# Kernel tuning notes

Hardware: AMD Instinct MI355X
Metric: run time of the kernel (lower is better)

The kernel has to match this reference:

```python
import jax, jax.numpy as jnp
import numpy as np

B, L, T = 16, 256, 256
ENC, DEC, MEL, SPK = 256, 1024, 80, 256
ATT, FILT, K = 128, 32, 31


def setup_inputs() -> dict:
    key = jax.random.key(0)
    ks = jax.random.split(key, 32)
    s = 0.05
    r = lambda k, shape: jax.random.normal(k, shape, dtype=jnp.float32) * s
    return {
        'encoder_outputs': jax.random.normal(ks[0], (B, L, ENC), dtype=jnp.float32),
        'speaker_embed': jax.random.normal(ks[1], (B, SPK), dtype=jnp.float32),
        'mels': jax.random.normal(ks[2], (B, T, MEL), dtype=jnp.float32),
        # prenet
        'W_pre1': r(ks[3], (DEC, MEL)), 'b_pre1': jnp.zeros((DEC,), jnp.float32),
        'W_pre2': r(ks[4], (DEC, DEC)), 'b_pre2': jnp.zeros((DEC,), jnp.float32),
        # speaker projection
        'W_sp': r(ks[5], (DEC, SPK)), 'b_sp': jnp.zeros((DEC,), jnp.float32),
        # location-sensitive attention (Tacotron-2 style)
        'W_q': r(ks[6], (ATT, DEC)),
        'W_m': r(ks[7], (ATT, ENC)),
        'W_loc_conv': r(ks[8], (FILT, 2, K)),
        'W_loc': r(ks[9], (ATT, FILT)),
        'v_att': r(ks[10], (ATT,)),
        # LSTM cells
        'W_ih1': r(ks[11], (4 * DEC, DEC + ENC)), 'W_hh1': r(ks[12], (4 * DEC, DEC)),
        'b_ih1': jnp.zeros((4 * DEC,), jnp.float32), 'b_hh1': jnp.zeros((4 * DEC,), jnp.float32),
        'W_ih2': r(ks[13], (4 * DEC, DEC)), 'W_hh2': r(ks[14], (4 * DEC, DEC)),
        'b_ih2': jnp.zeros((4 * DEC,), jnp.float32), 'b_hh2': jnp.zeros((4 * DEC,), jnp.float32),
        # output projections
        'W_mel': r(ks[15], (MEL, DEC)), 'b_mel': jnp.zeros((MEL,), jnp.float32),
        'W_stop': r(ks[16], (1, DEC)), 'b_stop': jnp.zeros((1,), jnp.float32),
    }


def _lstm_cell(x, h, c, W_ih, W_hh, b_ih, b_hh):
    g = x @ W_ih.T + h @ W_hh.T + b_ih + b_hh
    i, f, gg, o = jnp.split(g, 4, axis=-1)
    c2 = jax.nn.sigmoid(f) * c + jax.nn.sigmoid(i) * jnp.tanh(gg)
    h2 = jax.nn.sigmoid(o) * jnp.tanh(c2)
    return h2, c2


def reference(encoder_outputs, speaker_embed, mels,
              W_pre1, b_pre1, W_pre2, b_pre2, W_sp, b_sp,
              W_q, W_m, W_loc_conv, W_loc, v_att,
              W_ih1, W_hh1, b_ih1, b_hh1, W_ih2, W_hh2, b_ih2, b_hh2,
              W_mel, b_mel, W_stop, b_stop):
    b = encoder_outputs.shape[0]
    proc_mem = jnp.einsum('bld,ad->bla', encoder_outputs, W_m)  # [B,L,ATT]
    spk = speaker_embed @ W_sp.T + b_sp                          # [B,DEC]
    # teacher forcing: step 0 uses zeros, step i>0 uses mels[:, i] (matches torch loop)
    prev_mel_seq = jnp.concatenate([jnp.zeros_like(mels[:, :1]), mels[:, 1:]], axis=1)
    prev_mel_seq = prev_mel_seq.transpose(1, 0, 2)               # [T,B,MEL]

    def step(carry, prev_mel):
        h1, c1, h2, c2, prev_w, cum_w = carry
        # prenet (dropout = identity in eval)
        p = jax.nn.relu(prev_mel @ W_pre1.T + b_pre1)
        p = jax.nn.relu(p @ W_pre2.T + b_pre2)
        q = p + spk
        # location features over [prev, cumulative] attention weights
        loc = jnp.stack([prev_w, cum_w], axis=1)                 # [B,2,L]
        f = jax.lax.conv_general_dilated(loc, W_loc_conv, (1,), [(K // 2, K // 2)],
                                         dimension_numbers=('NCH', 'OIH', 'NCH'))  # [B,FILT,L]
        e = jnp.einsum('bla,a->bl', jnp.tanh((q @ W_q.T)[:, None, :]
                                             + jnp.einsum('bcl,ac->bla', f, W_loc)
                                             + proc_mem), v_att)  # [B,L]
        w = jax.nn.softmax(e, axis=1)
        ctx = jnp.einsum('bl,bld->bd', w, encoder_outputs)        # [B,ENC]
        h1n, c1n = _lstm_cell(jnp.concatenate([p, ctx], axis=1), h1, c1, W_ih1, W_hh1, b_ih1, b_hh1)
        h2n, c2n = _lstm_cell(h1n, h2, c2, W_ih2, W_hh2, b_ih2, b_hh2)
        mel = h2n @ W_mel.T + b_mel
        stop = jax.nn.sigmoid(h2n @ W_stop.T + b_stop)
        return (h1n, c1n, h2n, c2n, w, cum_w + w), (mel, stop)

    z = lambda d: jnp.zeros((b, d), jnp.float32)
    carry0 = (z(DEC), z(DEC), z(DEC), z(DEC), z(L), z(L))
    _, (mel_seq, stop_seq) = jax.lax.scan(step, carry0, prev_mel_seq)
    return mel_seq.transpose(1, 0, 2), stop_seq.transpose(1, 0, 2)
```

## Files before the change

### kernel.cpp

```cpp
#include <hip/hip_runtime.h>


namespace {

constexpr int TT = 256, BB = 16, LL = 256, MELD = 80, FILTD = 32, KC = 31;
constexpr int P1 = 2308;
constexpr int P2 = 2052;

typedef float f32x4 __attribute__((ext_vector_type(4)));

struct Args {
  const float *enc, *spe, *mels;
  const float *Wpre1, *bpre1, *Wpre2, *bpre2, *Wsp, *bsp;
  const float *Wq, *Wm, *Wconv, *Wloc, *vatt;
  const float *Wih1, *Whh1, *bih1, *bhh1;
  const float *Wih2, *Whh2, *bih2, *bhh2;
  const float *Wmel, *bmel, *Wstop, *bstop;
  float *p, *X, *qp2, *pm2, *prevmel;
  float *h1a, *h1b, *c1, *h2a, *h2b, *c2;
  float *cum, *wexp, *uctx, *pctx, *psum, *spkvec, *spkq;
  float *W81, *b81, *tmp;
  int *slots, *epoch, *pslots, *pepoch;
  float *out;
};

__device__ __forceinline__ float fast_tanh(float x) {
  float ax = fabsf(x);
  float e = __expf(-2.f * ax);
  float t = (1.f - e) / (1.f + e);
  return copysignf(t, x);
}
__device__ __forceinline__ float fast_sig(float x) { return 1.f / (1.f + __expf(-x)); }

__device__ __forceinline__ float cld1(const float* p) {
  float v;
  asm volatile("global_load_dword %0, %1, off sc0 sc1\n\ts_waitcnt vmcnt(0)"
               : "=v"(v) : "v"(p) : "memory");
  return v;
}
__device__ __forceinline__ int cldi(const int* p) {
  int v;
  asm volatile("global_load_dword %0, %1, off sc0 sc1\n\ts_waitcnt vmcnt(0)"
               : "=v"(v) : "v"(p) : "memory");
  return v;
}
__device__ __forceinline__ void cst1(float* p, float v) {
  asm volatile("global_store_dword %0, %1, off sc0 sc1" :: "v"(p), "v"(v) : "memory");
}
__device__ __forceinline__ void csti(int* p, int v) {
  asm volatile("global_store_dword %0, %1, off sc0 sc1" :: "v"(p), "v"(v) : "memory");
}
__device__ __forceinline__ void cld4(f32x4 d[4], const f32x4* q0, const f32x4* q1,
                                     const f32x4* q2, const f32x4* q3) {
  asm volatile(
      "global_load_dwordx4 %0, %4, off sc0 sc1\n\t"
      "global_load_dwordx4 %1, %5, off sc0 sc1\n\t"
      "global_load_dwordx4 %2, %6, off sc0 sc1\n\t"
      "global_load_dwordx4 %3, %7, off sc0 sc1\n\t"
      "s_waitcnt vmcnt(0)"
      : "=&v"(d[0]), "=&v"(d[1]), "=&v"(d[2]), "=&v"(d[3])
      : "v"(q0), "v"(q1), "v"(q2), "v"(q3)
      : "memory");
}
__device__ __forceinline__ void cld8(f32x4 d[8], const f32x4* q0, const f32x4* q1,
                                     const f32x4* q2, const f32x4* q3, const f32x4* q4,
                                     const f32x4* q5, const f32x4* q6, const f32x4* q7) {
  asm volatile(
      "global_load_dwordx4 %0, %8, off sc0 sc1\n\t"
      "global_load_dwordx4 %1, %9, off sc0 sc1\n\t"
      "global_load_dwordx4 %2, %10, off sc0 sc1\n\t"
      "global_load_dwordx4 %3, %11, off sc0 sc1\n\t"
      "global_load_dwordx4 %4, %12, off sc0 sc1\n\t"
      "global_load_dwordx4 %5, %13, off sc0 sc1\n\t"
      "global_load_dwordx4 %6, %14, off sc0 sc1\n\t"
      "global_load_dwordx4 %7, %15, off sc0 sc1\n\t"
      "s_waitcnt vmcnt(0)"
      : "=&v"(d[0]), "=&v"(d[1]), "=&v"(d[2]), "=&v"(d[3]),
        "=&v"(d[4]), "=&v"(d[5]), "=&v"(d[6]), "=&v"(d[7])
      : "v"(q0), "v"(q1), "v"(q2), "v"(q3), "v"(q4), "v"(q5), "v"(q6), "v"(q7)
      : "memory");
}
__device__ __forceinline__ void cld8d(float d[8], const float* q0, const float* q1,
                                      const float* q2, const float* q3, const float* q4,
                                      const float* q5, const float* q6, const float* q7) {
  asm volatile(
      "global_load_dword %0, %8, off sc0 sc1\n\t"
      "global_load_dword %1, %9, off sc0 sc1\n\t"
      "global_load_dword %2, %10, off sc0 sc1\n\t"
      "global_load_dword %3, %11, off sc0 sc1\n\t"
      "global_load_dword %4, %12, off sc0 sc1\n\t"
      "global_load_dword %5, %13, off sc0 sc1\n\t"
      "global_load_dword %6, %14, off sc0 sc1\n\t"
      "global_load_dword %7, %15, off sc0 sc1\n\t"
      "s_waitcnt vmcnt(0)"
      : "=&v"(d[0]), "=&v"(d[1]), "=&v"(d[2]), "=&v"(d[3]),
        "=&v"(d[4]), "=&v"(d[5]), "=&v"(d[6]), "=&v"(d[7])
      : "v"(q0), "v"(q1), "v"(q2), "v"(q3), "v"(q4), "v"(q5), "v"(q6), "v"(q7)
      : "memory");
}

__device__ __forceinline__ void gridbar(int* slots, int* epoch, int target) {
  __syncthreads();
  if (blockIdx.x == 0) {
    if (threadIdx.x == 0) csti(&slots[0], target);
    while (cldi(&slots[threadIdx.x * 32]) < target) __builtin_amdgcn_s_sleep(1);
    __syncthreads();
    if (threadIdx.x == 0) csti(epoch, target);
  } else {
    if (threadIdx.x == 0) {
      csti(&slots[blockIdx.x * 32], target);
      while (cldi(epoch) < target) __builtin_amdgcn_s_sleep(8);
    }
  }
  __syncthreads();
}

__global__ void k_init(float* base, int n) {
  int i = blockIdx.x * blockDim.x + threadIdx.x;
  if (i < n) base[i] = 0.f;
}

__global__ void k_setpsum(float* psum) {
  if (threadIdx.x < 16) psum[256 + threadIdx.x * 16] = 1.f;
}

__global__ void k_prevmel(Args a) {
  int i = blockIdx.x * blockDim.x + threadIdx.x;
  if (i >= TT * BB * MELD) return;
  int m = i % MELD;
  int tb = i / MELD;
  int b = tb & 15, t = tb >> 4;
  a.prevmel[i] = (t == 0) ? 0.f : a.mels[(b * TT + t) * MELD + m];
}

__global__ void k_spkvec(Args a) {
  int i = blockIdx.x * blockDim.x + threadIdx.x;
  if (i >= BB * 1024) return;
  int b = i >> 10, j = i & 1023;
  const float* x = a.spe + b * 256;
  const float* w = a.Wsp + j * 256;
  float s = a.bsp[j];
  for (int k = 0; k < 256; ++k) s += x[k] * w[k];
  a.spkvec[i] = s;
}

__global__ void k_spkq(Args a) {
  int i = blockIdx.x * blockDim.x + threadIdx.x;
  if (i >= BB * 128) return;
  int b = i >> 7, q = i & 127;
  const float* x = a.spkvec + b * 1024;
  const float* w = a.Wq + q * 1024;
  float s = 0.f;
  for (int k = 0; k < 1024; ++k) s += x[k] * w[k];
  a.spkq[i] = s;
}

__global__ void k_prep81(Args a) {
  int i = blockIdx.x * blockDim.x + threadIdx.x;
  if (i < 81 * 1024) {
    int r = i >> 10, k = i & 1023;
    a.W81[i] = (r < 80) ? a.Wmel[r * 1024 + k] : a.Wstop[k];
  }
  if (i < 81) a.b81[i] = (i < 80) ? a.bmel[i] : a.bstop[0];
}

__global__ __launch_bounds__(256) void k_gemm(const float* __restrict__ A,
                                              const float* __restrict__ Bm,
                                              const float* __restrict__ bias,
                                              float* __restrict__ C,
                                              int M, int N, int K, int act) {
  __shared__ __align__(16) float As[16][132];
  __shared__ __align__(16) float Bs[16][68];
  const int bm = blockIdx.y * 128, bn = blockIdx.x * 64;
  const int tid = threadIdx.x;
  const int tm = (tid >> 4) * 8, tn = (tid & 15) * 4;
  float acc[8][4] = {};
  for (int k0 = 0; k0 < K; k0 += 16) {
    for (int i = tid; i < 512; i += 256) {
      int m = i >> 2, kq = i & 3;
      float4 v = *(const float4*)(A + (size_t)(bm + m) * K + k0 + kq * 4);
      As[kq * 4 + 0][m] = v.x; As[kq * 4 + 1][m] = v.y;
      As[kq * 4 + 2][m] = v.z; As[kq * 4 + 3][m] = v.w;
    }
    {
      int m = tid >> 2, kq = tid & 3;
      float4 v = *(const float4*)(Bm + (size_t)(bn + m) * K + k0 + kq * 4);
      Bs[kq * 4 + 0][m] = v.x; Bs[kq * 4 + 1][m] = v.y;
      Bs[kq * 4 + 2][m] = v.z; Bs[kq * 4 + 3][m] = v.w;
    }
    __syncthreads();
#pragma unroll
    for (int kk = 0; kk < 16; ++kk) {
      float4 a0 = *(const float4*)&As[kk][tm];
      float4 a1 = *(const float4*)&As[kk][tm + 4];
      float4 b0 = *(const float4*)&Bs[kk][tn];
      float av[8] = {a0.x, a0.y, a0.z, a0.w, a1.x, a1.y, a1.z, a1.w};
      float bv[4] = {b0.x, b0.y, b0.z, b0.w};
#pragma unroll
      for (int i = 0; i < 8; ++i)
#pragma unroll
        for (int j = 0; j < 4; ++j) acc[i][j] += av[i] * bv[j];
    }
    __syncthreads();
  }
#pragma unroll
  for (int i = 0; i < 8; ++i)
#pragma unroll
    for (int j = 0; j < 4; ++j) {
      float v = acc[i][j];
      if (bias) v += bias[bn + tn + j];
      if (act == 1) v = fmaxf(v, 0.f);
      C[(size_t)(bm + tm + i) * N + bn + tn + j] = v;
    }
}

__global__ void k_pm_transpose(Args a) {
  int i = blockIdx.x * blockDim.x + threadIdx.x;
  if (i >= BB * 128 * LL) return;
  int l = i & 255;
  int rest = i >> 8;
  int q = rest & 127, b = rest >> 7;
  a.pm2[i] = a.X[(size_t)((b << 8) + l) * 128 + q];
}

__global__ void k_addspkq(Args a) {
  int i = blockIdx.x * blockDim.x + threadIdx.x;
  if (i >= TT * BB * 128) return;
  int q = i & 127, b = (i >> 7) & 15;
  a.qp2[i] += a.spkq[b * 128 + q];
}

__global__ __launch_bounds__(256, 1) void k_barprobe(Args a) {
  for (int t = 0; t < 512; ++t) gridbar(a.pslots, a.pepoch, t + 1);
}

__global__ __launch_bounds__(256, 1) void k_persist(Args a) {
  __shared__ __align__(16) float xs[16 * P1];
  __shared__ float gbuf[16][20];
  const int wg = blockIdx.x, tid = threadIdx.x;
  const int wv = tid >> 6, lane = tid & 63;
  const int d0 = wg * 4, kl = lane * 4;

  float4 wL1[9][4];
  float4 wL2[8][4];
#pragma unroll
  for (int q = 0; q < 4; ++q) {
    const int row = wv * 1024 + d0 + q;
    const float* rih1 = a.Wih1 + (size_t)row * 1280;
    const float* rhh1 = a.Whh1 + (size_t)row * 1024;
    const float* rih2 = a.Wih2 + (size_t)row * 1024;
    const float* rhh2 = a.Whh2 + (size_t)row * 1024;
#pragma unroll
    for (int kb = 0; kb < 9; ++kb)
      wL1[kb][q] = (kb < 5) ? *(const float4*)(rih1 + kb * 256 + kl)
                            : *(const float4*)(rhh1 + kb * 256 + kl - 1280);
#pragma unroll
    for (int kb = 0; kb < 8; ++kb)
      wL2[kb][q] = (kb < 4) ? *(const float4*)(rih2 + kb * 256 + kl)
                            : *(const float4*)(rhh2 + kb * 256 + kl - 1024);
  }
  const int row_r = wv * 1024 + d0 + (lane >> 4);
  const float bsum1 = a.bih1[row_r] + a.bhh1[row_r];
  const float bsum2 = a.bih2[row_r] + a.bhh2[row_r];

  for (int t = 0; t < 259; ++t) {
    const int cur = t & 1, prv = cur ^ 1;

    if (t < 256) {
      float* loc0 = xs;
      float* loc1 = xs + 64;
      float* F = xs + 128;
      float* expv = xs + 672;
      const int b = wg >> 4, c = wg & 15, l0 = c << 4;
      float sm;
      {
        const f32x4* ps4 = (const f32x4*)(a.psum + prv * 256 + b * 16);
        f32x4 pd[4];
        cld4(pd, ps4, ps4 + 1, ps4 + 2, ps4 + 3);
        sm = 0.f;
#pragma unroll
        for (int i = 0; i < 4; ++i) sm += pd[i][0] + pd[i][1] + pd[i][2] + pd[i][3];
      }
      const float inv_ps = 1.f / sm;
      if (tid < 64) {
        int lp = l0 - 16 + tid;
        bool ok = (lp >= 0 && lp < LL);
        float we = 0.f, cm = 0.f;
        if (ok) {
          we = cld1(a.wexp + prv * 4096 + b * 256 + lp) * inv_ps;
          cm = cld1(a.cum + prv * 4096 + b * 256 + lp);
        }
        loc0[tid] = we;
        loc1[tid] = ok ? (cm + we) : 0.f;
      }
      __syncthreads();
      if (tid < 16) cst1(a.cum + cur * 4096 + b * 256 + l0 + tid, loc1[16 + tid]);
      for (int idx = tid; idx < FILTD * 16; idx += 256) {
        int fc = idx >> 4, ll = idx & 15;
        const float* w = a.Wconv + fc * 62;
        float s = 0.f;
#pragma unroll
        for (int k = 0; k < KC; ++k) {
          s += w[k] * loc0[ll + k + 1];
          s += w[31 + k] * loc1[ll + k + 1];
        }
        F[fc * 17 + ll] = s;
      }
      __syncthreads();
      {
        const int ll = tid >> 4, ag = tid & 15;
        const int l = l0 + ll;
        const float* qpb = a.qp2 + (size_t)((t << 4) + b) * 128;
        const float* pmb = a.pm2 + (size_t)b * 128 * 256;
        float s = 0.f;
        for (int q = ag * 8; q < ag * 8 + 8; ++q) {
          float x = qpb[q] + pmb[q * 256 + l];
          const float* wl = a.Wloc + q * 32;
#pragma unroll
          for (int fc = 0; fc < FILTD; ++fc) x += wl[fc] * F[fc * 17 + ll];
          s += a.vatt[q] * fast_tanh(x);
        }
        s += __shfl_down(s, 8, 16);
        s += __shfl_down(s, 4, 16);
        s += __shfl_down(s, 2, 16);
        s += __shfl_down(s, 1, 16);
        if (ag == 0) {
          float ex = __expf(s);
          expv[ll] = ex;
          cst1(a.wexp + cur * 4096 + b * 256 + l, ex);
        }
      }
      __syncthreads();
      if (tid == 0) {
        float s = 0.f;
#pragma unroll
        for (int i = 0; i < 16; ++i) s += expv[i];
        cst1(a.psum + cur * 256 + b * 16 + c, s);
      }
      {
        float s = 0.f;
        const float* eb = a.enc + (size_t)((b << 8) + l0) * 256 + tid;
#pragma unroll
        for (int ll = 0; ll < 16; ++ll) s += expv[ll] * eb[ll * 256];
        cst1(a.pctx + cur * 65536 + (b * 16 + c) * 256 + tid, s);
      }
      __syncthreads();
    }

    if (wg < 16 && t >= 1 && t <= 256) {
      const int s = t - 1, par = s & 1, b = wg;
      float sm;
      {
        const f32x4* ps4 = (const f32x4*)(a.psum + par * 256 + b * 16);
        f32x4 pd[4];
        cld4(pd, ps4, ps4 + 1, ps4 + 2, ps4 + 3);
        sm = 0.f;
#pragma unroll
        for (int i = 0; i < 4; ++i) sm += pd[i][0] + pd[i][1] + pd[i][2] + pd[i][3];
      }
      const float inv = 1.f / sm;
      const float* pc = a.pctx + par * 65536 + b * 4096 + tid;
      float d[8];
      float acc = 0.f;
      cld8d(d, pc, pc + 256, pc + 512, pc + 768, pc + 1024, pc + 1280, pc + 1536,
            pc + 1792);
#pragma unroll
      for (int i = 0; i < 8; ++i) acc += d[i];
      cld8d(d, pc + 2048, pc + 2304, pc + 2560, pc + 2816, pc + 3072, pc + 3328,
            pc + 3584, pc + 3840);
#pragma unroll
      for (int i = 0; i < 8; ++i) acc += d[i];
      cst1(a.uctx + par * 4096 + b * 256 + tid, acc * inv);
    }

    if (t >= 2 && t <= 257) {
      const int s1 = t - 2;
      const float* pt = a.p + (size_t)s1 * 16384;
      const float* h1r = (s1 & 1) ? a.h1a : a.h1b;
      float* h1w = (s1 & 1) ? a.h1b : a.h1a;
      for (int k = 0; k < 16; ++k) {
        int i4 = tid + k * 256, b = i4 >> 8, kq = i4 & 255;
        *(f32x4*)(xs + b * P1 + kq * 4) = *(const f32x4*)(pt + (size_t)i4 * 4);
      }
      {
        const f32x4* q = (const f32x4*)(a.uctx + (size_t)(s1 & 1) * 4096);
        f32x4 d[4];
        cld4(d, q + tid, q + tid + 256, q + tid + 512, q + tid + 768);
#pragma unroll
        for (int k = 0; k < 4; ++k) {
          int i4 = tid + k * 256, b = i4 >> 6, kq = i4 & 63;
          *(f32x4*)(xs + b * P1 + 1024 + kq * 4) = d[k];
        }
      }
      {
        const f32x4* q = (const f32x4*)h1r;
        f32x4 d[8];
#pragma unroll
        for (int hb = 0; hb < 2; ++hb) {
          const f32x4* qq = q + tid + hb * 2048;
          cld8(d, qq, qq + 256, qq + 512, qq + 768, qq + 1024, qq + 1280, qq + 1536,
               qq + 1792);
#pragma unroll
          for (int k = 0; k < 8; ++k) {
            int i4 = tid + (hb * 8 + k) * 256, b = i4 >> 8, kq = i4 & 255;
            *(f32x4*)(xs + b * P1 + 1280 + kq * 4) = d[k];
          }
        }
      }
      __syncthreads();
      float acc[4][16];
#pragma unroll
      for (int q = 0; q < 4; ++q)
#pragma unroll
        for (int b = 0; b < 16; ++b) acc[q][b] = 0.f;
#pragma unroll
      for (int kb = 0; kb < 9; ++kb) {
        const float* xb = xs + kb * 256 + kl;
#pragma unroll
        for (int b = 0; b < 16; ++b) {
          float4 x4 = *(const float4*)(xb + b * P1);
#pragma unroll
          for (int q = 0; q < 4; ++q) {
            acc[q][b] += wL1[kb][q].x * x4.x;
            acc[q][b] += wL1[kb][q].y * x4.y;
            acc[q][b] += wL1[kb][q].z * x4.z;
            acc[q][b] += wL1[kb][q].w * x4.w;
          }
        }
      }
      __syncthreads();
      float* red = xs + wv * 4352;
#pragma unroll
      for (int q = 0; q < 4; ++q)
#pragma unroll
        for (int b = 0; b < 16; ++b) red[(q * 16 + b) * 68 + lane] = acc[q][b];
      __syncthreads();
      {
        const float* rr = xs + wv * 4352 + lane * 68;
        float4 s4 = {0.f, 0.f, 0.f, 0.f};
#pragma unroll
        for (int i = 0; i < 16; ++i) {
          float4 v = *(const float4*)(rr + i * 4);
          s4.x += v.x; s4.y += v.y; s4.z += v.z; s4.w += v.w;
        }
        gbuf[wv * 4 + (lane >> 4)][lane & 15] = s4.x + s4.y + s4.z + s4.w + bsum1;
      }
      __syncthreads();
      if (tid < 64) {
        int dd = tid >> 4, b = tid & 15;
        int d = d0 + dd;
        float gi = gbuf[0 + dd][b], gf = gbuf[4 + dd][b];
        float gg = gbuf[8 + dd][b], go = gbuf[12 + dd][b];
        float co = a.c1[b * 1024 + d];
        float cn = fast_sig(gf) * co + fast_sig(gi) * fast_tanh(gg);
        float hn = fast_sig(go) * fast_tanh(cn);
        a.c1[b * 1024 + d] = cn;
        cst1(h1w + b * 1024 + d, hn);
      }
      __syncthreads();
    }

    if (t >= 3) {
      const int s2 = t - 3;
      const float* h1s = (s2 & 1) ? a.h1b : a.h1a;
      const float* h2r = (s2 & 1) ? a.h2a : a.h2b;
      float* h2w = (s2 & 1) ? a.h2b : a.h2a;
      {
        f32x4 d[8];
        const f32x4* q1 = (const f32x4*)h1s;
        const f32x4* q2 = (const f32x4*)h2r;
#pragma unroll
        for (int hb = 0; hb < 2; ++hb) {
          const f32x4* qq = q1 + tid + hb * 2048;
          cld8(d, qq, qq + 256, qq + 512, qq + 768, qq + 1024, qq + 1280, qq + 1536,
               qq + 1792);
#pragma unroll
          for (int k = 0; k < 8; ++k) {
            int i4 = tid + (hb * 8 + k) * 256, b = i4 >> 8, kq = i4 & 255;
            *(f32x4*)(xs + b * P2 + kq * 4) = d[k];
          }
        }
#pragma unroll
        for (int hb = 0; hb < 2; ++hb) {
          const f32x4* qq = q2 + tid + hb * 2048;
          cld8(d, qq, qq + 256, qq + 512, qq + 768, qq + 1024, qq + 1280, qq + 1536,
               qq + 1792);
#pragma unroll
          for (int k = 0; k < 8; ++k) {
            int i4 = tid + (hb * 8 + k) * 256, b = i4 >> 8, kq = i4 & 255;
            *(f32x4*)(xs + b * P2 + 1024 + kq * 4) = d[k];
          }
        }
      }
      __syncthreads();
      float acc[4][16];
#pragma unroll
      for (int q = 0; q < 4; ++q)
#pragma unroll
        for (int b = 0; b < 16; ++b) acc[q][b] = 0.f;
#pragma unroll
      for (int kb = 0; kb < 8; ++kb) {
        const float* xb = xs + kb * 256 + kl;
#pragma unroll
        for (int b = 0; b < 16; ++b) {
          float4 x4 = *(const float4*)(xb + b * P2);
#pragma unroll
          for (int q = 0; q < 4; ++q) {
            acc[q][b] += wL2[kb][q].x * x4.x;
            acc[q][b] += wL2[kb][q].y * x4.y;
            acc[q][b] += wL2[kb][q].z * x4.z;
            acc[q][b] += wL2[kb][q].w * x4.w;
          }
        }
      }
      __syncthreads();
      float* red = xs + wv * 4352;
#pragma unroll
      for (int q = 0; q < 4; ++q)
#pragma unroll
        for (int b = 0; b < 16; ++b) red[(q * 16 + b) * 68 + lane] = acc[q][b];
      __syncthreads();
      {
        const float* rr = xs + wv * 4352 + lane * 68;
        float4 s4 = {0.f, 0.f, 0.f, 0.f};
#pragma unroll
        for (int i = 0; i < 16; ++i) {
          float4 v = *(const float4*)(rr + i * 4);
          s4.x += v.x; s4.y += v.y; s4.z += v.z; s4.w += v.w;
        }
        gbuf[wv * 4 + (lane >> 4)][lane & 15] = s4.x + s4.y + s4.z + s4.w + bsum2;
      }
      __syncthreads();
      if (tid < 64) {
        int dd = tid >> 4, b = tid & 15;
        int d = d0 + dd;
        float gi = gbuf[0 + dd][b], gf = gbuf[4 + dd][b];
        float gg = gbuf[8 + dd][b], go = gbuf[12 + dd][b];
        float co = a.c2[b * 1024 + d];
        float cn = fast_sig(gf) * co + fast_sig(gi) * fast_tanh(gg);
        float hn = fast_sig(go) * fast_tanh(cn);
        a.c2[b * 1024 + d] = cn;
        cst1(h2w + b * 1024 + d, hn);
        a.X[(size_t)(s2 * 16 + b) * 1024 + d] = hn;
      }
    }

    if (t < 258) gridbar(a.slots, a.epoch, t + 1);
  }
}

__global__ void k_finish(Args a) {
  int i = blockIdx.x * blockDim.x + threadIdx.x;
  if (i >= 4096 * 128) return;
  int col = i & 127, tb = i >> 7;
  int t = tb >> 4, b = tb & 15;
  float v = a.tmp[i];
  if (col < 80) a.out[(size_t)(b * 256 + t) * 80 + col] = v;
  else if (col == 80) a.out[327680 + b * 256 + t] = fast_sig(v);
}

}

extern "C" void kernel_launch(void* const* d_in, const int* in_sizes, int n_in,
                              void* d_out, int out_size, void* d_ws, size_t ws_size,
                              hipStream_t stream) {
  float* ws = (float*)d_ws;
  Args a;
  a.enc = (const float*)d_in[0];
  a.spe = (const float*)d_in[1];
  a.mels = (const float*)d_in[2];
  a.Wpre1 = (const float*)d_in[3];  a.bpre1 = (const float*)d_in[4];
  a.Wpre2 = (const float*)d_in[5];  a.bpre2 = (const float*)d_in[6];
  a.Wsp = (const float*)d_in[7];    a.bsp = (const float*)d_in[8];
  a.Wq = (const float*)d_in[9];     a.Wm = (const float*)d_in[10];
  a.Wconv = (const float*)d_in[11]; a.Wloc = (const float*)d_in[12];
  a.vatt = (const float*)d_in[13];
  a.Wih1 = (const float*)d_in[14];  a.Whh1 = (const float*)d_in[15];
  a.bih1 = (const float*)d_in[16];  a.bhh1 = (const float*)d_in[17];
  a.Wih2 = (const float*)d_in[18];  a.Whh2 = (const float*)d_in[19];
  a.bih2 = (const float*)d_in[20];  a.bhh2 = (const float*)d_in[21];
  a.Wmel = (const float*)d_in[22];  a.bmel = (const float*)d_in[23];
  a.Wstop = (const float*)d_in[24]; a.bstop = (const float*)d_in[25];

  a.p    = ws + 0;
  a.X    = ws + 4194304;
  a.qp2  = ws + 8388608;
  a.pm2  = ws + 8912896;
  float* st = ws + 9437184;
  a.h1a = st + 0;      a.h1b = st + 16384;
  a.c1  = st + 32768;
  a.h2a = st + 49152;  a.h2b = st + 65536;
  a.c2  = st + 81920;
  a.cum  = st + 98304;
  a.wexp = st + 106496;
  a.uctx = st + 114688;
  a.pctx = st + 122880;
  a.psum = st + 253952;
  a.slots  = (int*)(st + 254464);
  a.epoch  = (int*)(st + 262656);
  a.pslots = (int*)(st + 262688);
  a.pepoch = (int*)(st + 270880);
  a.spkvec = ws + 9708096;
  a.spkq   = ws + 9724480;
  a.W81    = ws + 9726528;
  a.b81    = ws + 9857600;
  a.tmp    = ws + 9857728;
  a.prevmel = a.tmp;
  a.out = (float*)d_out;

  k_init<<<(270912 + 255) / 256, 256, 0, stream>>>(st, 270912);
  k_setpsum<<<1, 64, 0, stream>>>(a.psum);
  k_prevmel<<<(TT * BB * MELD + 255) / 256, 256, 0, stream>>>(a);
  k_spkvec<<<(BB * 1024 + 255) / 256, 256, 0, stream>>>(a);
  k_spkq<<<(BB * 128 + 255) / 256, 256, 0, stream>>>(a);
  k_prep81<<<(81 * 1024 + 255) / 256, 256, 0, stream>>>(a);

  k_gemm<<<dim3(16, 32), 256, 0, stream>>>(a.prevmel, a.Wpre1, a.bpre1, a.X, 4096, 1024, 80, 1);
  k_gemm<<<dim3(16, 32), 256, 0, stream>>>(a.X, a.Wpre2, a.bpre2, a.p, 4096, 1024, 1024, 1);
  k_gemm<<<dim3(2, 32), 256, 0, stream>>>(a.p, a.Wq, nullptr, a.qp2, 4096, 128, 1024, 0);
  k_addspkq<<<(TT * BB * 128 + 255) / 256, 256, 0, stream>>>(a);
  k_gemm<<<dim3(2, 32), 256, 0, stream>>>(a.enc, a.Wm, nullptr, a.X, 4096, 128, 256, 0);
  k_pm_transpose<<<(BB * 128 * LL + 255) / 256, 256, 0, stream>>>(a);

  {
    void* kargs[] = {(void*)&a};
    hipError_t e = hipLaunchCooperativeKernel(reinterpret_cast<const void*>(&k_barprobe),
                                              dim3(256), dim3(256), kargs, 0, stream);
    if (e != hipSuccess) k_barprobe<<<256, 256, 0, stream>>>(a);
  }

  {
    void* kargs[] = {(void*)&a};
    hipError_t e = hipLaunchCooperativeKernel(reinterpret_cast<const void*>(&k_persist),
                                              dim3(256), dim3(256), kargs, 0, stream);
    if (e != hipSuccess) k_persist<<<256, 256, 0, stream>>>(a);
  }

  k_gemm<<<dim3(2, 32), 256, 0, stream>>>(a.X, a.W81, a.b81, a.tmp, 4096, 128, 1024, 0);
  k_finish<<<(4096 * 128 + 255) / 256, 256, 0, stream>>>(a);
}
```

Baseline: 14.00 ms.

## Restructure persistent decoder step: async LDS loads, register-resident state, shuffle reductions

Restructures the persistent per-step loop. Loads for the LSTM operands now go straight from global memory into LDS with global_load_lds, issued early so they overlap attention work. Attention constants (processed memory, v, encoder slice) and the LSTM cell states move into registers. The gate reductions switch from a padded LDS dump to wave shuffles plus a swizzled small reduction buffer, and many __syncthreads become lgkmcnt-wait barriers. It also removes the barrier probe kernel launch. In exchange it uses more registers and relies on padding-free LDS strides and carefully ordered waits.

```diff
diff --git a/kernel.cpp b/kernel.cpp
--- a/kernel.cpp
+++ b/kernel.cpp
@@ -4,8 +4,9 @@
 namespace {
 
 constexpr int TT = 256, BB = 16, LL = 256, MELD = 80, FILTD = 32, KC = 31;
-constexpr int P1 = 2308;
-constexpr int P2 = 2052;
+constexpr int P1 = 2304;
+constexpr int P2 = 2048;
+constexpr int REDOFF = 32768;
 
 typedef float f32x4 __attribute__((ext_vector_type(4)));
 
@@ -32,12 +33,6 @@
 }
 __device__ __forceinline__ float fast_sig(float x) { return 1.f / (1.f + __expf(-x)); }
 
-__device__ __forceinline__ float cld1(const float* p) {
-  float v;
-  asm volatile("global_load_dword %0, %1, off sc0 sc1\n\ts_waitcnt vmcnt(0)"
-               : "=v"(v) : "v"(p) : "memory");
-  return v;
-}
 __device__ __forceinline__ int cldi(const int* p) {
   int v;
   asm volatile("global_load_dword %0, %1, off sc0 sc1\n\ts_waitcnt vmcnt(0)"
@@ -49,6 +44,16 @@
 }
 __device__ __forceinline__ void csti(int* p, int v) {
   asm volatile("global_store_dword %0, %1, off sc0 sc1" :: "v"(p), "v"(v) : "memory");
+}
+__device__ __forceinline__ void cld2(float* d0, float* d1, const float* q0,
+                                     const float* q1) {
+  float x, y;
+  asm volatile(
+      "global_load_dword %0, %2, off sc0 sc1\n\t"
+      "global_load_dword %1, %3, off sc0 sc1\n\t"
+      "s_waitcnt vmcnt(0)"
+      : "=&v"(x), "=&v"(y) : "v"(q0), "v"(q1) : "memory");
+  *d0 = x; *d1 = y;
 }
 __device__ __forceinline__ void cld4(f32x4 d[4], const f32x4* q0, const f32x4* q1,
                                      const f32x4* q2, const f32x4* q3) {
@@ -60,24 +65,6 @@
       "s_waitcnt vmcnt(0)"
       : "=&v"(d[0]), "=&v"(d[1]), "=&v"(d[2]), "=&v"(d[3])
       : "v"(q0), "v"(q1), "v"(q2), "v"(q3)
-      : "memory");
-}
-__device__ __forceinline__ void cld8(f32x4 d[8], const f32x4* q0, const f32x4* q1,
-                                     const f32x4* q2, const f32x4* q3, const f32x4* q4,
-                                     const f32x4* q5, const f32x4* q6, const f32x4* q7) {
-  asm volatile(
-      "global_load_dwordx4 %0, %8, off sc0 sc1\n\t"
-      "global_load_dwordx4 %1, %9, off sc0 sc1\n\t"
-      "global_load_dwordx4 %2, %10, off sc0 sc1\n\t"
-      "global_load_dwordx4 %3, %11, off sc0 sc1\n\t"
-      "global_load_dwordx4 %4, %12, off sc0 sc1\n\t"
-      "global_load_dwordx4 %5, %13, off sc0 sc1\n\t"
-      "global_load_dwordx4 %6, %14, off sc0 sc1\n\t"
-      "global_load_dwordx4 %7, %15, off sc0 sc1\n\t"
-      "s_waitcnt vmcnt(0)"
-      : "=&v"(d[0]), "=&v"(d[1]), "=&v"(d[2]), "=&v"(d[3]),
-        "=&v"(d[4]), "=&v"(d[5]), "=&v"(d[6]), "=&v"(d[7])
-      : "v"(q0), "v"(q1), "v"(q2), "v"(q3), "v"(q4), "v"(q5), "v"(q6), "v"(q7)
       : "memory");
 }
 __device__ __forceinline__ void cld8d(float d[8], const float* q0, const float* q1,
@@ -99,6 +86,21 @@
       : "memory");
 }
 
+__device__ __forceinline__ void bar_lgkm() {
+  asm volatile("s_waitcnt lgkmcnt(0)" ::: "memory");
+  __builtin_amdgcn_s_barrier();
+  __builtin_amdgcn_sched_barrier(0);
+}
+
+__device__ __forceinline__ void glls_c(const float* g, float* l) {
+  __builtin_amdgcn_global_load_lds((const __attribute__((address_space(1))) void*)g,
+                                   (__attribute__((address_space(3))) void*)l, 16, 0, 17);
+}
+__device__ __forceinline__ void glls_p(const float* g, float* l) {
+  __builtin_amdgcn_global_load_lds((const __attribute__((address_space(1))) void*)g,
+                                   (__attribute__((address_space(3))) void*)l, 16, 0, 0);
+}
+
 __device__ __forceinline__ void gridbar(int* slots, int* epoch, int target) {
   __syncthreads();
   if (blockIdx.x == 0) {
@@ -230,16 +232,20 @@
   a.qp2[i] += a.spkq[b * 128 + q];
 }
 
-__global__ __launch_bounds__(256, 1) void k_barprobe(Args a) {
-  for (int t = 0; t < 512; ++t) gridbar(a.pslots, a.pepoch, t + 1);
-}
-
 __global__ __launch_bounds__(256, 1) void k_persist(Args a) {
   __shared__ __align__(16) float xs[16 * P1];
-  __shared__ float gbuf[16][20];
+  __shared__ __align__(16) float asc[720];
+  __shared__ __align__(16) float gbuf2[280];
+  __shared__ __align__(16) float wfb[2048];
   const int wg = blockIdx.x, tid = threadIdx.x;
   const int wv = tid >> 6, lane = tid & 63;
   const int d0 = wg * 4, kl = lane * 4;
+  const int ag = tid & 15, ll = tid >> 4;
+
+  float* loc0 = asc;
+  float* loc1 = asc + 64;
+  float* aF   = asc + 128;
+  float* expv = asc + 704;
 
   float4 wL1[9][4];
   float4 wL2[8][4];
@@ -263,62 +269,139 @@
   const float bsum1 = a.bih1[row_r] + a.bhh1[row_r];
   const float bsum2 = a.bih2[row_r] + a.bhh2[row_r];
 
+  const int bH = wg >> 4, cH = wg & 15, l0H = cH << 4, lH = l0H + ll;
+  float pmv[8], va[8];
+  {
+    const float* pmb = a.pm2 + (size_t)bH * 32768;
+#pragma unroll
+    for (int j = 0; j < 8; ++j) {
+      pmv[j] = pmb[(size_t)(ag * 8 + j) * 256 + lH];
+      va[j] = a.vatt[ag * 8 + j];
+    }
+  }
+  float ev[16];
+  {
+    const float* eb = a.enc + (size_t)((bH << 8) + l0H) * 256 + tid;
+#pragma unroll
+    for (int l2 = 0; l2 < 16; ++l2) ev[l2] = eb[l2 * 256];
+  }
+
+  float c1v = 0.f, c2v = 0.f;
+  __syncthreads();
+
   for (int t = 0; t < 259; ++t) {
     const int cur = t & 1, prv = cur ^ 1;
 
-    if (t < 256) {
-      float* loc0 = xs;
-      float* loc1 = xs + 64;
-      float* F = xs + 128;
-      float* expv = xs + 672;
-      const int b = wg >> 4, c = wg & 15, l0 = c << 4;
+    if (wg < 16 && t >= 1 && t <= 256) {
+      const int par = (t - 1) & 1, b = wg;
       float sm;
       {
-        const f32x4* ps4 = (const f32x4*)(a.psum + prv * 256 + b * 16);
+        const f32x4* ps4 = (const f32x4*)(a.psum + par * 256 + b * 16);
         f32x4 pd[4];
         cld4(pd, ps4, ps4 + 1, ps4 + 2, ps4 + 3);
         sm = 0.f;
 #pragma unroll
         for (int i = 0; i < 4; ++i) sm += pd[i][0] + pd[i][1] + pd[i][2] + pd[i][3];
       }
+      const float inv = 1.f / sm;
+      const float* pc = a.pctx + par * 65536 + b * 4096 + tid;
+      float d[8];
+      float acc = 0.f;
+      cld8d(d, pc, pc + 256, pc + 512, pc + 768, pc + 1024, pc + 1280, pc + 1536,
+            pc + 1792);
+#pragma unroll
+      for (int i = 0; i < 8; ++i) acc += d[i];
+      cld8d(d, pc + 2048, pc + 2304, pc + 2560, pc + 2816, pc + 3072, pc + 3328,
+            pc + 3584, pc + 3840);
+#pragma unroll
+      for (int i = 0; i < 8; ++i) acc += d[i];
+      cst1(a.uctx + par * 4096 + b * 256 + tid, acc * inv);
+    }
+
+    float qv[8];
+    if (t < 256) {
+      float sm;
+      {
+        const f32x4* ps4 = (const f32x4*)(a.psum + prv * 256 + bH * 16);
+        f32x4 pd[4];
+        cld4(pd, ps4, ps4 + 1, ps4 + 2, ps4 + 3);
+        sm = 0.f;
+#pragma unroll
+        for (int i = 0; i < 4; ++i) sm += pd[i][0] + pd[i][1] + pd[i][2] + pd[i][3];
+      }
       const float inv_ps = 1.f / sm;
+      {
+        const float* qpb = a.qp2 + ((size_t)(t << 4) + bH) * 128 + ag * 8;
+        *(float4*)&qv[0] = *(const float4*)qpb;
+        *(float4*)&qv[4] = *(const float4*)(qpb + 4);
+      }
       if (tid < 64) {
-        int lp = l0 - 16 + tid;
+        int lp = l0H - 16 + tid;
         bool ok = (lp >= 0 && lp < LL);
         float we = 0.f, cm = 0.f;
-        if (ok) {
-          we = cld1(a.wexp + prv * 4096 + b * 256 + lp) * inv_ps;
-          cm = cld1(a.cum + prv * 4096 + b * 256 + lp);
-        }
-        loc0[tid] = we;
-        loc1[tid] = ok ? (cm + we) : 0.f;
-      }
-      __syncthreads();
-      if (tid < 16) cst1(a.cum + cur * 4096 + b * 256 + l0 + tid, loc1[16 + tid]);
+        if (ok)
+          cld2(&we, &cm, a.wexp + prv * 4096 + bH * 256 + lp,
+               a.cum + prv * 4096 + bH * 256 + lp);
+        float wn = we * inv_ps;
+        loc0[tid] = wn;
+        loc1[tid] = ok ? (cm + wn) : 0.f;
+      }
+      bar_lgkm();
+      if (tid < 16) cst1(a.cum + cur * 4096 + bH * 256 + l0H + tid, loc1[16 + tid]);
       for (int idx = tid; idx < FILTD * 16; idx += 256) {
-        int fc = idx >> 4, ll = idx & 15;
+        int fc = idx >> 4, ll2 = idx & 15;
         const float* w = a.Wconv + fc * 62;
         float s = 0.f;
 #pragma unroll
         for (int k = 0; k < KC; ++k) {
-          s += w[k] * loc0[ll + k + 1];
-          s += w[31 + k] * loc1[ll + k + 1];
-        }
-        F[fc * 17 + ll] = s;
-      }
-      __syncthreads();
-      {
-        const int ll = tid >> 4, ag = tid & 15;
-        const int l = l0 + ll;
-        const float* qpb = a.qp2 + (size_t)((t << 4) + b) * 128;
-        const float* pmb = a.pm2 + (size_t)b * 128 * 256;
+          s += w[k] * loc0[ll2 + k + 1];
+          s += w[31 + k] * loc1[ll2 + k + 1];
+        }
+        aF[ll2 * 36 + fc] = s;
+      }
+      bar_lgkm();
+      {
+        const float* ftr = aF + ll * 36;
+#pragma unroll
+        for (int j = 0; j < 8; ++j) {
+          const int r = ag * 8 + j;
+          const float* wl = a.Wloc + r * 32;
+          float x = 0.f;
+#pragma unroll
+          for (int c4 = 0; c4 < 8; ++c4) {
+            float4 w4 = *(const float4*)(wl + c4 * 4);
+            f32x4 f4 = *(const f32x4*)(ftr + c4 * 4);
+            x += w4.x * f4[0] + w4.y * f4[1] + w4.z * f4[2] + w4.w * f4[3];
+          }
+          wfb[r * 16 + ll] = x;
+        }
+      }
+    }
+
+    if (t >= 2 && t <= 257) {
+      const int s1 = t - 2;
+      const float* pt = a.p + (size_t)s1 * 16384;
+      const float* h1r = (s1 & 1) ? a.h1a : a.h1b;
+      const float* uc = a.uctx + (size_t)(s1 & 1) * 4096;
+#pragma unroll
+      for (int k = 0; k < 16; ++k)
+        glls_p(pt + (size_t)(tid + k * 256) * 4, xs + k * P1 + wv * 256);
+#pragma unroll
+      for (int k = 0; k < 4; ++k)
+        glls_c(uc + (size_t)(tid + k * 256) * 4, xs + (k * 4 + wv) * P1 + 1024);
+#pragma unroll
+      for (int k = 0; k < 16; ++k)
+        glls_c(h1r + (size_t)(tid + k * 256) * 4, xs + k * P1 + 1280 + wv * 256);
+    }
+
+    if (t < 256) {
+      bar_lgkm();
+      {
         float s = 0.f;
-        for (int q = ag * 8; q < ag * 8 + 8; ++q) {
-          float x = qpb[q] + pmb[q * 256 + l];
-          const float* wl = a.Wloc + q * 32;
-#pragma unroll
-          for (int fc = 0; fc < FILTD; ++fc) x += wl[fc] * F[fc * 17 + ll];
-          s += a.vatt[q] * fast_tanh(x);
+#pragma unroll
+        for (int j = 0; j < 8; ++j) {
+          float x = qv[j] + pmv[j] + wfb[(ag * 8 + j) * 16 + ll];
+          s += va[j] * fast_tanh(x);
         }
         s += __shfl_down(s, 8, 16);
         s += __shfl_down(s, 4, 16);
@@ -327,86 +410,25 @@
         if (ag == 0) {
           float ex = __expf(s);
           expv[ll] = ex;
-          cst1(a.wexp + cur * 4096 + b * 256 + l, ex);
-        }
-      }
-      __syncthreads();
+          cst1(a.wexp + cur * 4096 + bH * 256 + lH, ex);
+        }
+      }
+      bar_lgkm();
       if (tid == 0) {
         float s = 0.f;
 #pragma unroll
         for (int i = 0; i < 16; ++i) s += expv[i];
-        cst1(a.psum + cur * 256 + b * 16 + c, s);
-      }
-      {
-        float s = 0.f;
-        const float* eb = a.enc + (size_t)((b << 8) + l0) * 256 + tid;
-#pragma unroll
-        for (int ll = 0; ll < 16; ++ll) s += expv[ll] * eb[ll * 256];
-        cst1(a.pctx + cur * 65536 + (b * 16 + c) * 256 + tid, s);
-      }
-      __syncthreads();
-    }
-
-    if (wg < 16 && t >= 1 && t <= 256) {
-      const int s = t - 1, par = s & 1, b = wg;
-      float sm;
-      {
-        const f32x4* ps4 = (const f32x4*)(a.psum + par * 256 + b * 16);
-        f32x4 pd[4];
-        cld4(pd, ps4, ps4 + 1, ps4 + 2, ps4 + 3);
-        sm = 0.f;
-#pragma unroll
-        for (int i = 0; i < 4; ++i) sm += pd[i][0] + pd[i][1] + pd[i][2] + pd[i][3];
-      }
-      const float inv = 1.f / sm;
-      const float* pc = a.pctx + par * 65536 + b * 4096 + tid;
-      float d[8];
-      float acc = 0.f;
-      cld8d(d, pc, pc + 256, pc + 512, pc + 768, pc + 1024, pc + 1280, pc + 1536,
-            pc + 1792);
-#pragma unroll
-      for (int i = 0; i < 8; ++i) acc += d[i];
-      cld8d(d, pc + 2048, pc + 2304, pc + 2560, pc + 2816, pc + 3072, pc + 3328,
-            pc + 3584, pc + 3840);
-#pragma unroll
-      for (int i = 0; i < 8; ++i) acc += d[i];
-      cst1(a.uctx + par * 4096 + b * 256 + tid, acc * inv);
+        cst1(a.psum + cur * 256 + bH * 16 + cH, s);
+      }
+      {
+        float sctx = 0.f;
+#pragma unroll
+        for (int l2 = 0; l2 < 16; ++l2) sctx += expv[l2] * ev[l2];
+        cst1(a.pctx + cur * 65536 + (bH * 16 + cH) * 256 + tid, sctx);
+      }
     }
 
     if (t >= 2 && t <= 257) {
-      const int s1 = t - 2;
-      const float* pt = a.p + (size_t)s1 * 16384;
-      const float* h1r = (s1 & 1) ? a.h1a : a.h1b;
-      float* h1w = (s1 & 1) ? a.h1b : a.h1a;
-      for (int k = 0; k < 16; ++k) {
-        int i4 = tid + k * 256, b = i4 >> 8, kq = i4 & 255;
-        *(f32x4*)(xs + b * P1 + kq * 4) = *(const f32x4*)(pt + (size_t)i4 * 4);
-      }
-      {
-        const f32x4* q = (const f32x4*)(a.uctx + (size_t)(s1 & 1) * 4096);
-        f32x4 d[4];
-        cld4(d, q + tid, q + tid + 256, q + tid + 512, q + tid + 768);
-#pragma unroll
-        for (int k = 0; k < 4; ++k) {
-          int i4 = tid + k * 256, b = i4 >> 6, kq = i4 & 63;
-          *(f32x4*)(xs + b * P1 + 1024 + kq * 4) = d[k];
-        }
-      }
-      {
-        const f32x4* q = (const f32x4*)h1r;
-        f32x4 d[8];
-#pragma unroll
-        for (int hb = 0; hb < 2; ++hb) {
-          const f32x4* qq = q + tid + hb * 2048;
-          cld8(d, qq, qq + 256, qq + 512, qq + 768, qq + 1024, qq + 1280, qq + 1536,
-               qq + 1792);
-#pragma unroll
-          for (int k = 0; k < 8; ++k) {
-            int i4 = tid + (hb * 8 + k) * 256, b = i4 >> 8, kq = i4 & 255;
-            *(f32x4*)(xs + b * P1 + 1280 + kq * 4) = d[k];
-          }
-        }
-      }
       __syncthreads();
       float acc[4][16];
 #pragma unroll
@@ -428,70 +450,67 @@
           }
         }
       }
-      __syncthreads();
-      float* red = xs + wv * 4352;
 #pragma unroll
       for (int q = 0; q < 4; ++q)
 #pragma unroll
-        for (int b = 0; b < 16; ++b) red[(q * 16 + b) * 68 + lane] = acc[q][b];
-      __syncthreads();
-      {
-        const float* rr = xs + wv * 4352 + lane * 68;
-        float4 s4 = {0.f, 0.f, 0.f, 0.f};
-#pragma unroll
-        for (int i = 0; i < 16; ++i) {
-          float4 v = *(const float4*)(rr + i * 4);
-          s4.x += v.x; s4.y += v.y; s4.z += v.z; s4.w += v.w;
-        }
-        gbuf[wv * 4 + (lane >> 4)][lane & 15] = s4.x + s4.y + s4.z + s4.w + bsum1;
-      }
-      __syncthreads();
-      if (tid < 64) {
-        int dd = tid >> 4, b = tid & 15;
-        int d = d0 + dd;
-        float gi = gbuf[0 + dd][b], gf = gbuf[4 + dd][b];
-        float gg = gbuf[8 + dd][b], go = gbuf[12 + dd][b];
-        float co = a.c1[b * 1024 + d];
-        float cn = fast_sig(gf) * co + fast_sig(gi) * fast_tanh(gg);
-        float hn = fast_sig(go) * fast_tanh(cn);
-        a.c1[b * 1024 + d] = cn;
-        cst1(h1w + b * 1024 + d, hn);
-      }
-      __syncthreads();
-    }
+        for (int b = 0; b < 16; ++b) {
+          float v = acc[q][b];
+          v += __shfl_xor(v, 32);
+          v += __shfl_xor(v, 16);
+          acc[q][b] = v;
+        }
+      if (lane < 16) {
+        float* rb = xs + REDOFF + wv * 1024 + lane * 64;
+        const int sx = lane << 2;
+#pragma unroll
+        for (int q = 0; q < 4; ++q)
+#pragma unroll
+          for (int bg = 0; bg < 4; ++bg) {
+            f32x4 v = {acc[q][bg * 4 + 0], acc[q][bg * 4 + 1],
+                       acc[q][bg * 4 + 2], acc[q][bg * 4 + 3]};
+            *(f32x4*)(rb + ((q * 16 + bg * 4) ^ sx)) = v;
+          }
+      }
+    }
+    bar_lgkm();
 
     if (t >= 3) {
       const int s2 = t - 3;
       const float* h1s = (s2 & 1) ? a.h1b : a.h1a;
       const float* h2r = (s2 & 1) ? a.h2a : a.h2b;
+#pragma unroll
+      for (int k = 0; k < 16; ++k)
+        glls_c(h1s + (size_t)(tid + k * 256) * 4, xs + k * P2 + wv * 256);
+#pragma unroll
+      for (int k = 0; k < 16; ++k)
+        glls_c(h2r + (size_t)(tid + k * 256) * 4, xs + k * P2 + 1024 + wv * 256);
+    }
+
+    if (t >= 2 && t <= 257) {
+      float* h1w = ((t - 2) & 1) ? a.h1b : a.h1a;
+      {
+        const int lo = lane & ~3, li = lane & 3;
+        const float* rbase = xs + REDOFF + wv * 1024;
+        float g = bsum1;
+#pragma unroll
+        for (int k = 0; k < 16; ++k) g += rbase[k * 64 + (lo ^ (k << 2)) + li];
+        gbuf2[wv * 68 + lane] = g;
+      }
+      bar_lgkm();
+      if (tid < 64) {
+        int dd = tid >> 4, b = tid & 15, d = d0 + dd;
+        float gi = gbuf2[0 * 68 + tid], gf = gbuf2[1 * 68 + tid];
+        float gg = gbuf2[2 * 68 + tid], go = gbuf2[3 * 68 + tid];
+        float cn = fast_sig(gf) * c1v + fast_sig(gi) * fast_tanh(gg);
+        float hn = fast_sig(go) * fast_tanh(cn);
+        c1v = cn;
+        cst1(h1w + b * 1024 + d, hn);
+      }
+    }
+
+    if (t >= 3) {
+      const int s2 = t - 3;
       float* h2w = (s2 & 1) ? a.h2b : a.h2a;
-      {
-        f32x4 d[8];
-        const f32x4* q1 = (const f32x4*)h1s;
-        const f32x4* q2 = (const f32x4*)h2r;
-#pragma unroll
-        for (int hb = 0; hb < 2; ++hb) {
-          const f32x4* qq = q1 + tid + hb * 2048;
-          cld8(d, qq, qq + 256, qq + 512, qq + 768, qq + 1024, qq + 1280, qq + 1536,
-               qq + 1792);
-#pragma unroll
-          for (int k = 0; k < 8; ++k) {
-            int i4 = tid + (hb * 8 + k) * 256, b = i4 >> 8, kq = i4 & 255;
-            *(f32x4*)(xs + b * P2 + kq * 4) = d[k];
-          }
-        }
-#pragma unroll
-        for (int hb = 0; hb < 2; ++hb) {
-          const f32x4* qq = q2 + tid + hb * 2048;
-          cld8(d, qq, qq + 256, qq + 512, qq + 768, qq + 1024, qq + 1280, qq + 1536,
-               qq + 1792);
-#pragma unroll
-          for (int k = 0; k < 8; ++k) {
-            int i4 = tid + (hb * 8 + k) * 256, b = i4 >> 8, kq = i4 & 255;
-            *(f32x4*)(xs + b * P2 + 1024 + kq * 4) = d[k];
-          }
-        }
-      }
       __syncthreads();
       float acc[4][16];
 #pragma unroll
@@ -513,33 +532,44 @@
           }
         }
       }
-      __syncthreads();
-      float* red = xs + wv * 4352;
 #pragma unroll
       for (int q = 0; q < 4; ++q)
 #pragma unroll
-        for (int b = 0; b < 16; ++b) red[(q * 16 + b) * 68 + lane] = acc[q][b];
-      __syncthreads();
-      {
-        const float* rr = xs + wv * 4352 + lane * 68;
-        float4 s4 = {0.f, 0.f, 0.f, 0.f};
-#pragma unroll
-        for (int i = 0; i < 16; ++i) {
-          float4 v = *(const float4*)(rr + i * 4);
-          s4.x += v.x; s4.y += v.y; s4.z += v.z; s4.w += v.w;
-        }
-        gbuf[wv * 4 + (lane >> 4)][lane & 15] = s4.x + s4.y + s4.z + s4.w + bsum2;
-      }
-      __syncthreads();
+        for (int b = 0; b < 16; ++b) {
+          float v = acc[q][b];
+          v += __shfl_xor(v, 32);
+          v += __shfl_xor(v, 16);
+          acc[q][b] = v;
+        }
+      if (lane < 16) {
+        float* rb = xs + REDOFF + wv * 1024 + lane * 64;
+        const int sx = lane << 2;
+#pragma unroll
+        for (int q = 0; q < 4; ++q)
+#pragma unroll
+          for (int bg = 0; bg < 4; ++bg) {
+            f32x4 v = {acc[q][bg * 4 + 0], acc[q][bg * 4 + 1],
+                       acc[q][bg * 4 + 2], acc[q][bg * 4 + 3]};
+            *(f32x4*)(rb + ((q * 16 + bg * 4) ^ sx)) = v;
+          }
+      }
+      bar_lgkm();
+      {
+        const int lo = lane & ~3, li = lane & 3;
+        const float* rbase = xs + REDOFF + wv * 1024;
+        float g = bsum2;
+#pragma unroll
+        for (int k = 0; k < 16; ++k) g += rbase[k * 64 + (lo ^ (k << 2)) + li];
+        gbuf2[wv * 68 + lane] = g;
+      }
+      bar_lgkm();
       if (tid < 64) {
-        int dd = tid >> 4, b = tid & 15;
-        int d = d0 + dd;
-        float gi = gbuf[0 + dd][b], gf = gbuf[4 + dd][b];
-        float gg = gbuf[8 + dd][b], go = gbuf[12 + dd][b];
-        float co = a.c2[b * 1024 + d];
-        float cn = fast_sig(gf) * co + fast_sig(gi) * fast_tanh(gg);
+        int dd = tid >> 4, b = tid & 15, d = d0 + dd;
+        float gi = gbuf2[0 * 68 + tid], gf = gbuf2[1 * 68 + tid];
+        float gg = gbuf2[2 * 68 + tid], go = gbuf2[3 * 68 + tid];
+        float cn = fast_sig(gf) * c2v + fast_sig(gi) * fast_tanh(gg);
         float hn = fast_sig(go) * fast_tanh(cn);
-        a.c2[b * 1024 + d] = cn;
+        c2v = cn;
         cst1(h2w + b * 1024 + d, hn);
         a.X[(size_t)(s2 * 16 + b) * 1024 + d] = hn;
       }
@@ -624,13 +654,6 @@
 
   {
     void* kargs[] = {(void*)&a};
-    hipError_t e = hipLaunchCooperativeKernel(reinterpret_cast<const void*>(&k_barprobe),
-                                              dim3(256), dim3(256), kargs, 0, stream);
-    if (e != hipSuccess) k_barprobe<<<256, 256, 0, stream>>>(a);
-  }
-
-  {
-    void* kargs[] = {(void*)&a};
     hipError_t e = hipLaunchCooperativeKernel(reinterpret_cast<const void*>(&k_persist),
                                               dim3(256), dim3(256), kargs, 0, stream);
     if (e != hipSuccess) k_persist<<<256, 256, 0, stream>>>(a);
```

Measured after the change: 14.30 ms. 2.1% more time.
